# Optimization experiments

Hardware: AMD Instinct MI355X
Metric: run time of the kernel (lower is better)

## Reference

```python
import jax, jax.numpy as jnp
import numpy as np

WS = 512            # window_size
STEP = WS // 2      # hop
K = WS // 2 + 1     # rfft coeffs = 257


def hann(n):
    # periodic hann window (matches torch.hann_window default)
    return 0.5 * (1.0 - jnp.cos(2.0 * jnp.pi * jnp.arange(n) / n))


def setup_inputs() -> dict:
    key = jax.random.key(0)
    k1, k2, k3 = jax.random.split(key, 3)
    B, C, T = 4, 64, 65536
    x = jax.random.normal(k1, (B, C, T), dtype=jnp.float32)
    # mixer initialized near identity (nn.Parameter(torch.eye(C)) after some training)
    mixer = jnp.eye(C, dtype=jnp.float32) + 0.01 * jax.random.normal(k2, (C, C), dtype=jnp.float32)
    # stable per-coefficient transfer magnitudes in [0, 0.9)
    transfer = jax.random.uniform(k3, (C, K), dtype=jnp.float32) * 0.9
    gain = jnp.full((1,), 1.5, dtype=jnp.float32)
    return {"x": x, "mixer": mixer, "transfer": transfer, "gain": gain}


def reference(x, mixer, transfer, gain):
    B, C, T = x.shape
    # (x^T @ mixer)^T
    x = jnp.einsum('bct,cd->bdt', x, mixer)
    # windowed_audio: pad by hop, unfold into half-overlapping frames
    xp = jnp.pad(x, ((0, 0), (0, 0), (0, STEP)))
    n_frames = (xp.shape[-1] - WS) // STEP + 1
    idx = jnp.arange(n_frames)[:, None] * STEP + jnp.arange(WS)[None, :]  # [F, WS]
    windowed = xp[:, :, idx]                     # [B, C, F, WS]
    spec = jnp.fft.rfft(windowed, axis=-1)       # [B, C, F, K] complex64
    # linear recurrence over frames: y_i = (spec_i + y_{i-1}) * transfer
    def step(carry, s):
        y = (s + carry) * transfer[None]         # [B, C, K]
        return y, y
    spec_t = jnp.transpose(spec, (2, 0, 1, 3))   # [F, B, C, K]
    y0 = jnp.zeros((B, C, K), dtype=spec.dtype)
    _, ys = jax.lax.scan(step, y0, spec_t)       # [F, B, C, K]
    out_spec = jnp.transpose(ys, (1, 2, 0, 3))   # [B, C, F, K]
    # inverse FFT + windowed overlap-add
    aw = jnp.fft.irfft(out_spec, n=WS, axis=-1)  # [B, C, F, WS]
    aw = aw * hann(WS)[None, None, None, :]
    L = (n_frames - 1) * STEP + WS
    samples = jnp.zeros((B, C, L), dtype=aw.dtype).at[:, :, idx].add(aw)
    samples = jnp.tanh(samples * gain[0])
    return samples[..., :T]
```

## Files before the change

kernel.cpp:

```cpp
#include <hip/hip_runtime.h>
#include <math.h>

#define T_LEN  65536
#define T_PAD  65792
#define C_CH   64
#define STEP_  256
#define K_     257
#define NW     16
#define NIT    16

#define SW(i) ((i) ^ (((i) >> 2) & 12))

#define CFENCE() asm volatile("" ::: "memory")
#define BAR() do { asm volatile("s_waitcnt lgkmcnt(0)" ::: "memory"); \
                   __builtin_amdgcn_s_barrier(); \
                   asm volatile("" ::: "memory"); } while (0)

__device__ __forceinline__ float2 cadd(float2 a, float2 b) { return make_float2(a.x + b.x, a.y + b.y); }
__device__ __forceinline__ float2 csub(float2 a, float2 b) { return make_float2(a.x - b.x, a.y - b.y); }
__device__ __forceinline__ float2 cmul(float2 a, float2 b) {
    return make_float2(a.x * b.x - a.y * b.y, a.x * b.y + a.y * b.x);
}
template <int SGN>
__device__ __forceinline__ float2 cmulsg(float2 w, float2 t) {
    if (SGN > 0) return make_float2(w.x * t.x - w.y * t.y, w.x * t.y + w.y * t.x);
    else         return make_float2(w.x * t.x + w.y * t.y, w.x * t.y - w.y * t.x);
}
template <int SGN>
__device__ __forceinline__ void bfly4(float2 z0, float2 z1, float2 z2, float2 z3,
                                      float2& o0, float2& o1, float2& o2, float2& o3,
                                      float2 w1, float2 w2, float2 w3) {
    float2 apc = cadd(z0, z2), amc = csub(z0, z2);
    float2 bpd = cadd(z1, z3), bmd = csub(z1, z3);
    float2 jb  = make_float2(-bmd.y, bmd.x);
    float2 t1, t3;
    if (SGN > 0) { t1 = csub(amc, jb); t3 = cadd(amc, jb); }
    else         { t1 = cadd(amc, jb); t3 = csub(amc, jb); }
    o0 = cadd(apc, bpd);
    o1 = cmulsg<SGN>(w1, t1);
    o2 = cmulsg<SGN>(w2, csub(apc, bpd));
    o3 = cmulsg<SGN>(w3, t3);
}
template <int SGN>
__device__ __forceinline__ void bfly4nt(float2 z0, float2 z1, float2 z2, float2 z3,
                                        float2& o0, float2& o1, float2& o2, float2& o3) {
    float2 apc = cadd(z0, z2), amc = csub(z0, z2);
    float2 bpd = cadd(z1, z3), bmd = csub(z1, z3);
    float2 jb  = make_float2(-bmd.y, bmd.x);
    o0 = cadd(apc, bpd);
    o2 = csub(apc, bpd);
    if (SGN > 0) { o1 = csub(amc, jb); o3 = cadd(amc, jb); }
    else         { o1 = cadd(amc, jb); o3 = csub(amc, jb); }
}

__device__ __forceinline__ float ftanh(float x) {
    float e = __expf(2.0f * x);
    return 1.0f - 2.0f * __builtin_amdgcn_rcpf(e + 1.0f);
}

__global__ __launch_bounds__(512, 1) void mix_kernel(const float* __restrict__ x,
                                                     const float* __restrict__ mixer,
                                                     float* __restrict__ mixed) {
    __shared__ __align__(16) float xt[64][128];
    __shared__ __align__(16) float mx[64][64];
    int tid = threadIdx.x;
    int b   = blockIdx.y;
    int t0  = blockIdx.x * 128;

    if (t0 >= T_LEN) {
        for (int f = tid; f < 8192; f += 512) {
            int d = f >> 7, tt = f & 127;
            mixed[((size_t)(b * C_CH + d)) * T_PAD + t0 + tt] = 0.0f;
        }
        return;
    }
    for (int f = tid; f < 4096; f += 512) reinterpret_cast<float*>(mx)[f] = mixer[f];
    for (int f4 = tid; f4 < 2048; f4 += 512) {
        int cc = f4 >> 5, tt4 = f4 & 31;
        *reinterpret_cast<float4*>(&xt[cc][tt4 * 4]) =
            *reinterpret_cast<const float4*>(&x[((size_t)(b * C_CH + cc)) * T_LEN + t0 + tt4 * 4]);
    }
    __syncthreads();

    int tp = tid & 63, grp = tid >> 6;
    int dbase = grp * 8;
    float2 acc[8];
#pragma unroll
    for (int i = 0; i < 8; ++i) acc[i] = make_float2(0.0f, 0.0f);
    for (int cc = 0; cc < 64; ++cc) {
        float2 xv = *reinterpret_cast<const float2*>(&xt[cc][2 * tp]);
        float4 m0 = *reinterpret_cast<const float4*>(&mx[cc][dbase + 0]);
        float4 m1 = *reinterpret_cast<const float4*>(&mx[cc][dbase + 4]);
        acc[0].x = fmaf(xv.x, m0.x, acc[0].x); acc[0].y = fmaf(xv.y, m0.x, acc[0].y);
        acc[1].x = fmaf(xv.x, m0.y, acc[1].x); acc[1].y = fmaf(xv.y, m0.y, acc[1].y);
        acc[2].x = fmaf(xv.x, m0.z, acc[2].x); acc[2].y = fmaf(xv.y, m0.z, acc[2].y);
        acc[3].x = fmaf(xv.x, m0.w, acc[3].x); acc[3].y = fmaf(xv.y, m0.w, acc[3].y);
        acc[4].x = fmaf(xv.x, m1.x, acc[4].x); acc[4].y = fmaf(xv.y, m1.x, acc[4].y);
        acc[5].x = fmaf(xv.x, m1.y, acc[5].x); acc[5].y = fmaf(xv.y, m1.y, acc[5].y);
        acc[6].x = fmaf(xv.x, m1.z, acc[6].x); acc[6].y = fmaf(xv.y, m1.z, acc[6].y);
        acc[7].x = fmaf(xv.x, m1.w, acc[7].x); acc[7].y = fmaf(xv.y, m1.w, acc[7].y);
    }
#pragma unroll
    for (int i = 0; i < 8; ++i)
        *reinterpret_cast<float2*>(&mixed[((size_t)(b * C_CH + dbase + i)) * T_PAD + t0 + 2 * tp]) = acc[i];
}

__global__ __launch_bounds__(1024, 4) void stft_kernel(const float* __restrict__ mixed,
                                                       const float* __restrict__ transfer,
                                                       const float* __restrict__ gainp,
                                                       float* __restrict__ out) {
    __shared__ __align__(16) float2 buf[NW][256];
    __shared__ __align__(16) float2 spec[2][NW][257];
    __shared__ __align__(16) float  olab[NW][264];
    __shared__ __align__(16) float  tails[2][264];

    const int tid  = threadIdx.x;
    const int bc   = blockIdx.x;
    const int b    = bc >> 6, c = bc & 63;
    const int g    = tid >> 6, lane = tid & 63;

    const float* src = mixed + ((size_t)(b * C_CH + c)) * T_PAD;
    float*       dst = out   + ((size_t)(b * C_CH + c)) * T_LEN;

    float2 pf0, pf1, pf2, pf3;
    {
        const float* fp = src + (size_t)g * STEP_;
        pf0 = *reinterpret_cast<const float2*>(fp + 2 * lane);
        pf1 = *reinterpret_cast<const float2*>(fp + 2 * (lane + 64));
        pf2 = *reinterpret_cast<const float2*>(fp + 2 * (lane + 128));
        pf3 = *reinterpret_cast<const float2*>(fp + 2 * (lane + 192));
    }

    const float TWO_PI = 6.2831853071795864f;
    float sn, cn;
    sincosf(TWO_PI * (float)lane / 256.0f, &sn, &cn);
    const float2 w1a = make_float2(cn, -sn), w2a = cmul(w1a, w1a), w3a = cmul(w2a, w1a);
    sincosf(TWO_PI * (float)(lane >> 2) / 64.0f, &sn, &cn);
    const float2 w1b = make_float2(cn, -sn), w2b = cmul(w1b, w1b), w3b = cmul(w2b, w1b);
    sincosf(TWO_PI * (float)(lane >> 4) / 16.0f, &sn, &cn);
    const float2 w1c = make_float2(cn, -sn), w2c = cmul(w1c, w1c), w3c = cmul(w2c, w1c);
    float2 wh[4];
#pragma unroll
    for (int qq = 0; qq < 4; ++qq) {
        sincosf(3.14159265358979f * (float)(lane + 64 * qq) / 256.0f, &sn, &cn);
        wh[qq] = make_float2(cn, -sn);
    }
#define HV(m) ((0.5f - 0.5f * cosf(TWO_PI * (float)(m) / 512.0f)) * (1.0f / 512.0f))
    const float h0 = HV(2 * lane),       h1 = HV(2 * lane + 1);
    const float h2 = HV(2 * lane + 128), h3 = HV(2 * lane + 129);
    const float h4 = HV(2 * lane + 256), h5 = HV(2 * lane + 257);
    const float h6 = HV(2 * lane + 384), h7 = HV(2 * lane + 385);
#undef HV

    const int q2  = (lane & 3)  + ((lane >> 2) << 4);
    const int q3  = (lane & 15) + ((lane >> 4) << 6);
    const int swl = SW(lane);
    const int s1b = (4 * lane) ^ (lane & 12);
    const int sq2a = SW(q2);
    const int sq2b = SW(q2 + 4);
    const int sq2c = SW(q2 + 8);
    const int sq2d = SW(q2 + 12);
    const int sq3a = q3;
    const int sq3b = (q3 + 16) ^ 4;
    const int sq3c = (q3 + 32) ^ 8;
    const int sq3d = (q3 + 48) ^ 12;
    const int mm0 = SW((256 - lane) & 255);
    const int mm1 = SW(192 - lane);
    const int mm2 = SW(128 - lane);
    const int mm3 = SW(64 - lane);

    int sk = -1;
    if (g < 4) sk = (g << 6) | lane;
    else if (g == 4 && lane == 0) sk = 256;
    float  tk = 0.0f;
    float2 yc = make_float2(0.0f, 0.0f);
    if (sk >= 0) tk = transfer[c * K_ + sk];

    if (tid < 256) tails[0][tid] = 0.0f;
    const float gv = gainp[0];
    float2* bin = &buf[g][0];
    BAR();

    for (int it = 0; it <= NIT; ++it) {
        const int sp = it & 1;
        if (it < NIT) {
            const int f = it * NW + g;
            float2 z0 = pf0, z1 = pf1, z2 = pf2, z3 = pf3;
            if (it + 1 < NIT) {
                const float* fp = src + (size_t)(f + NW) * STEP_;
                pf0 = *reinterpret_cast<const float2*>(fp + 2 * lane);
                pf1 = *reinterpret_cast<const float2*>(fp + 2 * (lane + 64));
                pf2 = *reinterpret_cast<const float2*>(fp + 2 * (lane + 128));
                pf3 = *reinterpret_cast<const float2*>(fp + 2 * (lane + 192));
            }
            float2 o0, o1, o2, o3;
            bfly4<1>(z0, z1, z2, z3, o0, o1, o2, o3, w1a, w2a, w3a);
            {
                float2* bw = bin + s1b;
                *reinterpret_cast<float4*>(bw)     = make_float4(o0.x, o0.y, o1.x, o1.y);
                *reinterpret_cast<float4*>(bw + 2) = make_float4(o2.x, o2.y, o3.x, o3.y);
            }
            CFENCE();
            z0 = bin[swl]; z1 = bin[swl + 64]; z2 = bin[swl + 128]; z3 = bin[swl + 192];
            bfly4<1>(z0, z1, z2, z3, o0, o1, o2, o3, w1b, w2b, w3b);
            CFENCE();
            bin[sq2a] = o0; bin[sq2b] = o1; bin[sq2c] = o2; bin[sq2d] = o3;
            CFENCE();
            z0 = bin[swl]; z1 = bin[swl + 64]; z2 = bin[swl + 128]; z3 = bin[swl + 192];
            bfly4<1>(z0, z1, z2, z3, o0, o1, o2, o3, w1c, w2c, w3c);
            CFENCE();
            bin[sq3a] = o0; bin[sq3b] = o1; bin[sq3c] = o2; bin[sq3d] = o3;
            CFENCE();
            z0 = bin[swl]; z1 = bin[swl + 64]; z2 = bin[swl + 128]; z3 = bin[swl + 192];
            bfly4nt<1>(z0, z1, z2, z3, o0, o1, o2, o3);
            CFENCE();
            bin[swl] = o0; bin[swl + 64] = o1; bin[swl + 128] = o2; bin[swl + 192] = o3;
            CFENCE();
            {
                float2 v0 = bin[mm0], v1 = bin[mm1], v2 = bin[mm2], v3 = bin[mm3];
                float2 uu[4] = {o0, o1, o2, o3}, vv[4] = {v0, v1, v2, v3};
#pragma unroll
                for (int qq = 0; qq < 4; ++qq) {
                    int k = lane + 64 * qq;
                    float2 E = make_float2(0.5f * (uu[qq].x + vv[qq].x),  0.5f * (uu[qq].y - vv[qq].y));
                    float2 O = make_float2(0.5f * (uu[qq].y + vv[qq].y), -0.5f * (uu[qq].x - vv[qq].x));
                    spec[sp][g][k] = cadd(E, cmul(wh[qq], O));
                }
                if (lane == 0) spec[sp][g][256] = make_float2(o0.x - o0.y, 0.0f);
            }
        }
        BAR();
        if (it < NIT && sk >= 0) {
            float2* s0 = &spec[sp][0][sk];
            float2 v[8]; float2 y = yc;
#pragma unroll
            for (int gg = 0; gg < 8; ++gg) v[gg] = s0[gg * 257];
#pragma unroll
            for (int gg = 0; gg < 8; ++gg) {
                y.x = (v[gg].x + y.x) * tk; y.y = (v[gg].y + y.y) * tk;
                s0[gg * 257] = y;
            }
#pragma unroll
            for (int gg = 0; gg < 8; ++gg) v[gg] = s0[(gg + 8) * 257];
#pragma unroll
            for (int gg = 0; gg < 8; ++gg) {
                y.x = (v[gg].x + y.x) * tk; y.y = (v[gg].y + y.y) * tk;
                s0[(gg + 8) * 257] = y;
            }
            yc = y;
        }
        if (it > 0) {
            const int fb = (it - 1) * NW + g;
            const float2* specP = &spec[sp ^ 1][g][0];
            float2 o0, o1, o2, o3;
            {
                float2 iu[4], is_[4];
                iu[0] = specP[lane];       is_[0] = specP[256 - lane];
                iu[1] = specP[lane + 64];  is_[1] = specP[192 - lane];
                iu[2] = specP[lane + 128]; is_[2] = specP[128 - lane];
                iu[3] = specP[lane + 192]; is_[3] = specP[64 - lane];
                float2 zz[4];
#pragma unroll
                for (int qq = 0; qq < 4; ++qq) {
                    float2 A  = make_float2(iu[qq].x + is_[qq].x, iu[qq].y - is_[qq].y);
                    float2 D  = make_float2(iu[qq].x - is_[qq].x, iu[qq].y + is_[qq].y);
                    float2 Bv = cmulsg<-1>(wh[qq], D);
                    zz[qq] = make_float2(A.x - Bv.y, A.y + Bv.x);
                }
                bfly4<-1>(zz[0], zz[1], zz[2], zz[3], o0, o1, o2, o3, w1a, w2a, w3a);
            }
            {
                float2* bw = bin + s1b;
                *reinterpret_cast<float4*>(bw)     = make_float4(o0.x, o0.y, o1.x, o1.y);
                *reinterpret_cast<float4*>(bw + 2) = make_float4(o2.x, o2.y, o3.x, o3.y);
            }
            CFENCE();
            float2 z0 = bin[swl], z1 = bin[swl + 64], z2 = bin[swl + 128], z3 = bin[swl + 192];
            bfly4<-1>(z0, z1, z2, z3, o0, o1, o2, o3, w1b, w2b, w3b);
            CFENCE();
            bin[sq2a] = o0; bin[sq2b] = o1; bin[sq2c] = o2; bin[sq2d] = o3;
            CFENCE();
            z0 = bin[swl]; z1 = bin[swl + 64]; z2 = bin[swl + 128]; z3 = bin[swl + 192];
            bfly4<-1>(z0, z1, z2, z3, o0, o1, o2, o3, w1c, w2c, w3c);
            CFENCE();
            bin[sq3a] = o0; bin[sq3b] = o1; bin[sq3c] = o2; bin[sq3d] = o3;
            CFENCE();
            z0 = bin[swl]; z1 = bin[swl + 64]; z2 = bin[swl + 128]; z3 = bin[swl + 192];
            bfly4nt<-1>(z0, z1, z2, z3, o0, o1, o2, o3);
            {
                float2 sh0 = make_float2(o2.x * h4, o2.y * h5);
                float2 sh1 = make_float2(o3.x * h6, o3.y * h7);
                float* wrow = (g == NW - 1) ? tails[it & 1] : olab[g + 1];
                *reinterpret_cast<float2*>(&wrow[2 * lane])       = sh0;
                *reinterpret_cast<float2*>(&wrow[2 * lane + 128]) = sh1;
            }
            BAR();
            {
                const float* prow = (g == 0) ? tails[(it - 1) & 1] : olab[g];
                float2 p0 = *reinterpret_cast<const float2*>(&prow[2 * lane]);
                float2 p1 = *reinterpret_cast<const float2*>(&prow[2 * lane + 128]);
                float2 r0 = make_float2(ftanh((o0.x * h0 + p0.x) * gv),
                                        ftanh((o0.y * h1 + p0.y) * gv));
                float2 r1 = make_float2(ftanh((o1.x * h2 + p1.x) * gv),
                                        ftanh((o1.y * h3 + p1.y) * gv));
                float* dp = dst + (size_t)fb * STEP_;
                *reinterpret_cast<float2*>(&dp[2 * lane])       = r0;
                *reinterpret_cast<float2*>(&dp[2 * lane + 128]) = r1;
            }
        }
    }
}

extern "C" void kernel_launch(void* const* d_in, const int* in_sizes, int n_in,
                              void* d_out, int out_size, void* d_ws, size_t ws_size,
                              hipStream_t stream) {
    (void)in_sizes; (void)n_in; (void)out_size; (void)ws_size;
    const float* x        = (const float*)d_in[0];
    const float* mixer    = (const float*)d_in[1];
    const float* transfer = (const float*)d_in[2];
    const float* gain     = (const float*)d_in[3];
    float* out   = (float*)d_out;
    float* mixed = (float*)d_ws;

    dim3 gmix(T_PAD / 128, 4);
    mix_kernel<<<gmix, 512, 0, stream>>>(x, mixer, mixed);
    stft_kernel<<<256, 1024, 0, stream>>>(mixed, transfer, gain, out);
}
```

Before: 114.1 us.

## Defer overlap-add output by one iteration to remove a per-iteration barrier

The overlap-add and tanh output stage now runs one loop iteration later. The current frame's own half is kept in registers, while the neighbour halves go into double-buffered olab and quad-buffered tails arrays. The barrier that used to sit between the inverse-FFT write and the read now lives in the next iteration's existing barriers, so the extra barrier per iteration is gone. In exchange it adds an extra loop iteration, more shared memory (which may lower occupancy), and some register pressure.

```diff
diff --git a/kernel.cpp b/kernel.cpp
--- a/kernel.cpp
+++ b/kernel.cpp
@@ -111,8 +111,8 @@
                                                        float* __restrict__ out) {
     __shared__ __align__(16) float2 buf[NW][256];
     __shared__ __align__(16) float2 spec[2][NW][257];
-    __shared__ __align__(16) float  olab[NW][264];
-    __shared__ __align__(16) float  tails[2][264];
+    __shared__ __align__(16) float  olab2[2][NW][264];
+    __shared__ __align__(16) float  tails[4][264];
 
     const int tid  = threadIdx.x;
     const int bc   = blockIdx.x;
@@ -176,18 +176,18 @@
     float2 yc = make_float2(0.0f, 0.0f);
     if (sk >= 0) tk = transfer[c * K_ + sk];
 
-    if (tid < 256) tails[0][tid] = 0.0f;
+    if (tid < 256) tails[3][tid] = 0.0f;
     const float gv = gainp[0];
     float2* bin = &buf[g][0];
+    float2 sval0 = make_float2(0.f, 0.f), sval1 = make_float2(0.f, 0.f);
     BAR();
 
-    for (int it = 0; it <= NIT; ++it) {
+    for (int it = 0; it <= NIT + 1; ++it) {
         const int sp = it & 1;
         if (it < NIT) {
-            const int f = it * NW + g;
             float2 z0 = pf0, z1 = pf1, z2 = pf2, z3 = pf3;
             if (it + 1 < NIT) {
-                const float* fp = src + (size_t)(f + NW) * STEP_;
+                const float* fp = src + (size_t)((it + 1) * NW + g) * STEP_;
                 pf0 = *reinterpret_cast<const float2*>(fp + 2 * lane);
                 pf1 = *reinterpret_cast<const float2*>(fp + 2 * (lane + 64));
                 pf2 = *reinterpret_cast<const float2*>(fp + 2 * (lane + 128));
@@ -249,8 +249,8 @@
             }
             yc = y;
         }
-        if (it > 0) {
-            const int fb = (it - 1) * NW + g;
+        float2 nv0, nv1;
+        if (it >= 1 && it <= NIT) {
             const float2* specP = &spec[sp ^ 1][g][0];
             float2 o0, o1, o2, o3;
             {
@@ -290,24 +290,29 @@
             {
                 float2 sh0 = make_float2(o2.x * h4, o2.y * h5);
                 float2 sh1 = make_float2(o3.x * h6, o3.y * h7);
-                float* wrow = (g == NW - 1) ? tails[it & 1] : olab[g + 1];
+                float* wrow = (g == NW - 1) ? tails[(it - 1) & 3] : olab2[(it - 1) & 1][g + 1];
                 *reinterpret_cast<float2*>(&wrow[2 * lane])       = sh0;
                 *reinterpret_cast<float2*>(&wrow[2 * lane + 128]) = sh1;
             }
-            BAR();
-            {
-                const float* prow = (g == 0) ? tails[(it - 1) & 1] : olab[g];
-                float2 p0 = *reinterpret_cast<const float2*>(&prow[2 * lane]);
-                float2 p1 = *reinterpret_cast<const float2*>(&prow[2 * lane + 128]);
-                float2 r0 = make_float2(ftanh((o0.x * h0 + p0.x) * gv),
-                                        ftanh((o0.y * h1 + p0.y) * gv));
-                float2 r1 = make_float2(ftanh((o1.x * h2 + p1.x) * gv),
-                                        ftanh((o1.y * h3 + p1.y) * gv));
-                float* dp = dst + (size_t)fb * STEP_;
-                *reinterpret_cast<float2*>(&dp[2 * lane])       = r0;
-                *reinterpret_cast<float2*>(&dp[2 * lane + 128]) = r1;
-            }
-        }
+            nv0 = make_float2(o0.x * h0, o0.y * h1);
+            nv1 = make_float2(o1.x * h2, o1.y * h3);
+        } else {
+            nv0 = make_float2(0.f, 0.f); nv1 = make_float2(0.f, 0.f);
+        }
+        if (it >= 2) {
+            const int fs = (it - 2) * NW + g;
+            const float* prow = (g == 0) ? tails[(it - 3) & 3] : olab2[(it - 2) & 1][g];
+            float2 p0 = *reinterpret_cast<const float2*>(&prow[2 * lane]);
+            float2 p1 = *reinterpret_cast<const float2*>(&prow[2 * lane + 128]);
+            float2 r0 = make_float2(ftanh((sval0.x + p0.x) * gv),
+                                    ftanh((sval0.y + p0.y) * gv));
+            float2 r1 = make_float2(ftanh((sval1.x + p1.x) * gv),
+                                    ftanh((sval1.y + p1.y) * gv));
+            float* dp = dst + (size_t)fs * STEP_;
+            *reinterpret_cast<float2*>(&dp[2 * lane])       = r0;
+            *reinterpret_cast<float2*>(&dp[2 * lane + 128]) = r1;
+        }
+        sval0 = nv0; sval1 = nv1;
     }
 }
 
```

New measurement: 115.5 us. Within noise of the previous version (+1.2%).
